# Kernel tuning notes

Measured on AMD Instinct MI355X. Metric: run time of the kernel, lower is better.

Reference implementation:

```python
import jax, jax.numpy as jnp
import numpy as np

B = 4; C = 3; IMG = 256; P = 16; HP = 16; HW = 256
DIM = 512; DEPTH = 6; HEADS = 8; DH = 64
NS = 50; SH = 4; SDH = 64; ITERS = 3; RPD = 128; FF = 2048; N = NS + HW


def _ln(x, g, b):
    m = jnp.mean(x, -1, keepdims=True)
    v = jnp.var(x, -1, keepdims=True)
    return (x - m) * jax.lax.rsqrt(v + 1e-5) * g + b


def _rms(x, g):
    # lucidrains RMSNorm: F.normalize(x, dim=-1) * sqrt(dim) * gamma
    n = jnp.linalg.norm(x, axis=-1, keepdims=True)
    return x / jnp.maximum(n, 1e-12) * (DIM ** 0.5) * g


def setup_inputs() -> dict:
    key = jax.random.key(0)
    ks = iter(jax.random.split(key, 64))
    def W(*s):
        return jax.random.normal(next(ks), s, jnp.float32) * 0.02
    SI = SH * SDH
    d = {}
    d['images'] = jax.random.normal(next(ks), (B, C, IMG, IMG), jnp.float32)
    d['slot_noise'] = jax.random.normal(next(ks), (B, NS, DIM), jnp.float32)
    d['patch_w'] = W(C * P * P, DIM); d['patch_b'] = jnp.zeros((DIM,))
    d['hpos'] = W(HP, DIM); d['wpos'] = W(HP, DIM)
    d['rp_w1'] = W(2, RPD); d['rp_b1'] = jnp.zeros((RPD,))
    d['rp_w2'] = W(RPD, RPD); d['rp_b2'] = jnp.zeros((RPD,))
    d['rp_w3'] = W(RPD, HEADS); d['rp_b3'] = jnp.zeros((HEADS,))
    d['slots_mu'] = W(1, 1, DIM); d['slots_logsigma'] = jnp.zeros((1, 1, DIM))
    d['sa_ln_in_g'] = jnp.ones((DIM,)); d['sa_ln_in_b'] = jnp.zeros((DIM,))
    d['sa_ln_sl_g'] = jnp.ones((DIM,)); d['sa_ln_sl_b'] = jnp.zeros((DIM,))
    d['sa_wq'] = W(DIM, SI); d['sa_bq'] = jnp.zeros((SI,))
    d['sa_wk'] = W(DIM, SI); d['sa_bk'] = jnp.zeros((SI,))
    d['sa_wv'] = W(DIM, SI); d['sa_bv'] = jnp.zeros((SI,))
    d['sa_wo'] = W(SI, DIM); d['sa_bo'] = jnp.zeros((DIM,))
    d['gru_wih'] = W(DIM, 3 * DIM); d['gru_whh'] = W(DIM, 3 * DIM)
    d['gru_bih'] = jnp.zeros((3 * DIM,)); d['gru_bhh'] = jnp.zeros((3 * DIM,))
    d['sa_ln_ff_g'] = jnp.ones((DIM,)); d['sa_ln_ff_b'] = jnp.zeros((DIM,))
    d['sa_mlp_w1'] = W(DIM, DIM); d['sa_mlp_b1'] = jnp.zeros((DIM,))
    d['sa_mlp_w2'] = W(DIM, DIM); d['sa_mlp_b2'] = jnp.zeros((DIM,))
    d['s2c_w'] = W(DIM, 2); d['s2c_b'] = jnp.zeros((2,))
    d['attn_g'] = jnp.ones((DEPTH, DIM))
    d['wq'] = W(DEPTH, DIM, HEADS * DH); d['wk'] = W(DEPTH, DIM, HEADS * DH)
    d['wv'] = W(DEPTH, DIM, HEADS * DH); d['wo'] = W(DEPTH, HEADS * DH, DIM)
    d['ff_g'] = jnp.ones((DEPTH, DIM))
    d['ff_w1'] = W(DEPTH, DIM, FF); d['ff_b1'] = jnp.zeros((DEPTH, FF))
    d['ff_w2'] = W(DEPTH, FF, DIM); d['ff_b2'] = jnp.zeros((DEPTH, DIM))
    d['final_g'] = jnp.ones((DIM,))
    d['pred_w'] = W(DIM, DIM); d['pred_b'] = jnp.zeros((DIM,))
    return d


def reference(images, slot_noise, patch_w, patch_b, hpos, wpos,
              rp_w1, rp_b1, rp_w2, rp_b2, rp_w3, rp_b3,
              slots_mu, slots_logsigma, sa_ln_in_g, sa_ln_in_b, sa_ln_sl_g, sa_ln_sl_b,
              sa_wq, sa_bq, sa_wk, sa_bk, sa_wv, sa_bv, sa_wo, sa_bo,
              gru_wih, gru_whh, gru_bih, gru_bhh, sa_ln_ff_g, sa_ln_ff_b,
              sa_mlp_w1, sa_mlp_b1, sa_mlp_w2, sa_mlp_b2, s2c_w, s2c_b,
              attn_g, wq, wk, wv, wo, ff_g, ff_w1, ff_b1, ff_w2, ff_b2,
              final_g, pred_w, pred_b):
    b = images.shape[0]
    # patchify: b c (h p1) (w p2) -> b h w (p1 p2 c)
    x = images.reshape(b, C, HP, P, HP, P).transpose(0, 2, 4, 3, 5, 1).reshape(b, HP, HP, P * P * C)
    tokens = x @ patch_w + patch_b                     # [b, HP, HP, DIM]
    tokens = tokens + hpos[:, None, :] + wpos[None, :, :]
    tokens = tokens.reshape(b, HW, DIM)
    # --- multi-head slot attention ---
    inp = _ln(tokens, sa_ln_in_g, sa_ln_in_b)
    k = (inp @ sa_wk + sa_bk).reshape(b, HW, SH, SDH).transpose(0, 2, 1, 3)
    v = (inp @ sa_wv + sa_bv).reshape(b, HW, SH, SDH).transpose(0, 2, 1, 3)
    slots = slots_mu + jnp.exp(slots_logsigma) * slot_noise  # [b, NS, DIM]
    scale = SDH ** -0.5
    for _ in range(ITERS):
        prev = slots
        s = _ln(slots, sa_ln_sl_g, sa_ln_sl_b)
        q = (s @ sa_wq + sa_bq).reshape(b, NS, SH, SDH).transpose(0, 2, 1, 3)
        dots = jnp.einsum('bhid,bhjd->bhij', q, k) * scale     # [b, SH, NS, HW]
        attn = jax.nn.softmax(dots, axis=-2) + 1e-8            # softmax over slots
        attn = attn / jnp.sum(attn, -1, keepdims=True)         # weighted mean over inputs
        upd = jnp.einsum('bhij,bhjd->bhid', attn, v)
        upd = upd.transpose(0, 2, 1, 3).reshape(b, NS, SH * SDH) @ sa_wo + sa_bo
        # GRUCell(updates, prev_slots)
        gx = upd @ gru_wih + gru_bih
        gh = prev @ gru_whh + gru_bhh
        xr, xz, xn = jnp.split(gx, 3, -1)
        hr, hz, hn = jnp.split(gh, 3, -1)
        r = jax.nn.sigmoid(xr + hr)
        z = jax.nn.sigmoid(xz + hz)
        nn_ = jnp.tanh(xn + r * hn)
        slots = (1 - z) * nn_ + z * prev
        slots = slots + (jax.nn.relu(_ln(slots, sa_ln_ff_g, sa_ln_ff_b) @ sa_mlp_w1 + sa_mlp_b1) @ sa_mlp_w2 + sa_mlp_b2)
    objects = slots
    slot_coords = objects @ s2c_w + s2c_b              # [b, NS, 2]
    # --- relative position MLP bias (slots coords + patch grid) ---
    g = jnp.arange(HP, dtype=jnp.float32)
    grid = jnp.stack(jnp.meshgrid(g, g, indexing='ij'), -1).reshape(HW, 2)
    coords = jnp.concatenate([slot_coords, jnp.broadcast_to(grid, (b, HW, 2))], axis=1)  # [b, N, 2]
    rel = coords[:, :, None, :] - coords[:, None, :, :]   # [b, N, N, 2]
    hmid = jax.nn.silu(rel @ rp_w1 + rp_b1)
    hmid = jax.nn.silu(hmid @ rp_w2 + rp_b2)
    bias = jnp.transpose(hmid @ rp_w3 + rp_b3, (0, 3, 1, 2))  # [b, HEADS, N, N]
    # --- transformer with per-layer rel-pos bias ---
    x = jnp.concatenate([objects, tokens], axis=1)     # [b, N, DIM]
    ascale = DH ** -0.5
    for l in range(DEPTH):
        h = _rms(x, attn_g[l])
        qh = (h @ wq[l]).reshape(b, N, HEADS, DH).transpose(0, 2, 1, 3)
        kh = (h @ wk[l]).reshape(b, N, HEADS, DH).transpose(0, 2, 1, 3)
        vh = (h @ wv[l]).reshape(b, N, HEADS, DH).transpose(0, 2, 1, 3)
        sim = jnp.einsum('bhid,bhjd->bhij', qh, kh) * ascale + bias
        a = jax.nn.softmax(sim, -1)
        o = jnp.einsum('bhij,bhjd->bhid', a, vh).transpose(0, 2, 1, 3).reshape(b, N, HEADS * DH) @ wo[l]
        x = x + o
        h = _rms(x, ff_g[l])
        x = x + (jax.nn.gelu(h @ ff_w1[l] + ff_b1[l]) @ ff_w2[l] + ff_b2[l])
    x = _rms(x, final_g)
    return x[:, NS:] @ pred_w + pred_b                 # [b, HW, DIM]
```

## Files before the change

kernel.cpp:

```cpp
#include <hip/hip_runtime.h>
#include <hip/hip_bf16.h>

typedef __hip_bfloat16 bf16;
typedef short short8v __attribute__((ext_vector_type(8)));
typedef float float4v __attribute__((ext_vector_type(4)));

static __device__ __forceinline__ float b2f(bf16 x){ return __bfloat162float(x); }

static __device__ __forceinline__ float ldin(const void* p, size_t i, bool isbf) {
  return isbf ? b2f(((const bf16*)p)[i]) : ((const float*)p)[i];
}

static __device__ __forceinline__ unsigned short f2bu(float f) {
  bf16 h = __float2bfloat16(f);
  return *reinterpret_cast<unsigned short*>(&h);
}

#define CDIV(a,b) (((a)+(b)-1)/(b))

#define NB   4
#define NSL  50
#define HWT  256
#define NT   306
#define DIM  512
// ... 46 lines not shown
  __shared__ unsigned short S[64 * 72];
  int t = threadIdx.x;
  int kk = t >> 4, nn = (t & 15) * 4;
#pragma unroll
  for (int r = 0; r < 4; ++r) {
    int k = k0 + kk + r * 16;
    unsigned short v[4];
    if (isbf) {
      ushort4 u = *(const ushort4*)((const unsigned short*)W + slice + (size_t)k * N + n0 + nn);
      v[0]=u.x; v[1]=u.y; v[2]=u.z; v[3]=u.w;
    } else {
      float4 f = *(const float4*)((const float*)W + slice + (size_t)k * N + n0 + nn);
      v[0]=f2bu(f.x); v[1]=f2bu(f.y); v[2]=f2bu(f.z); v[3]=f2bu(f.w);
    }
#pragma unroll
    for (int i = 0; i < 4; ++i) S[(nn + i) * 72 + kk + r * 16] = v[i];
  }
  __syncthreads();
  int nr = t >> 2, kc = (t & 3) * 16;
  short8v s0 = *(const short8v*)&S[nr * 72 + kc];
  short8v s1 = *(const short8v*)&S[nr * 72 + kc + 8];
  unsigned short* dst = dst0 + slice + (size_t)(n0 + nr) * K + k0 + kc;
  *(short8v*)dst = s0;
  *(short8v*)(dst + 8) = s1;
}

#define LDK 72
static __device__ __forceinline__ void gemm_body2(
    const void* __restrict__ A, int aty,
    const unsigned short* __restrict__ WT,
    const void* __restrict__ bias, size_t boff,
    void* __restrict__ C, int oty,
    int M, int N, int K, int kbeg, int kend,
    int act, int mode, bool isbf)
{
  __shared__ unsigned short As[64 * LDK];
  __shared__ unsigned short Bs[64 * LDK];
  const int tid = threadIdx.x;
  const int lane = tid & 63, wave = tid >> 6;
  const int quad = lane >> 4, ti = lane & 15;
  const int wm = (wave & 1) * 32, wn = (wave >> 1) * 32;
  const int bm = blockIdx.y * 64, bn = blockIdx.x * 64;
  const int srow = tid >> 2, sch = (tid & 3) * 16;

  unsigned short ha[16], hb[16];
  const int gm = bm + srow;
  const bool aok = gm < M;
  const unsigned short* Abf = (const unsigned short*)A + (size_t)gm * K;
  const float*          Af  = (const float*)A + (size_t)gm * K;
  const unsigned short* Bp  = WT + (size_t)(bn + srow) * K;

  auto fetchA = [&](int k0) {
    if (aok) {
      if (aty) {
        const ushort4* ap = (const ushort4*)(Abf + k0 + sch);
#pragma unroll
        for (int i = 0; i < 4; ++i) {
          ushort4 u = ap[i];
          ha[i*4+0]=u.x; ha[i*4+1]=u.y; ha[i*4+2]=u.z; ha[i*4+3]=u.w;
        }
      } else {
        const float4* ap = (const float4*)(Af + k0 + sch);
#pragma unroll
        for (int i = 0; i < 4; ++i) {
          float4 f = ap[i];
          ha[i*4+0]=f2bu(f.x); ha[i*4+1]=f2bu(f.y); ha[i*4+2]=f2bu(f.z); ha[i*4+3]=f2bu(f.w);
        }
// ... 25 lines not shown
    for (int ks = 0; ks < 2; ++ks) {
      short8v a0 = *reinterpret_cast<const short8v*>(&As[(wm + ti)      * LDK + ks * 32 + quad * 8]);
      short8v a1 = *reinterpret_cast<const short8v*>(&As[(wm + 16 + ti) * LDK + ks * 32 + quad * 8]);
      short8v b0 = *reinterpret_cast<const short8v*>(&Bs[(wn + ti)      * LDK + ks * 32 + quad * 8]);
      short8v b1 = *reinterpret_cast<const short8v*>(&Bs[(wn + 16 + ti) * LDK + ks * 32 + quad * 8]);
      acc00 = __builtin_amdgcn_mfma_f32_16x16x32_bf16(a0, b0, acc00, 0, 0, 0);
      acc01 = __builtin_amdgcn_mfma_f32_16x16x32_bf16(a0, b1, acc01, 0, 0, 0);
      acc10 = __builtin_amdgcn_mfma_f32_16x16x32_bf16(a1, b0, acc10, 0, 0, 0);
      acc11 = __builtin_amdgcn_mfma_f32_16x16x32_bf16(a1, b1, acc11, 0, 0, 0);
    }
    __syncthreads();
  }

  float4v accs[2][2] = {{acc00, acc01}, {acc10, acc11}};
#pragma unroll
  for (int mi = 0; mi < 2; ++mi) {
#pragma unroll
    for (int ni = 0; ni < 2; ++ni) {
      int row0 = bm + wm + mi * 16 + quad * 4;
      int col  = bn + wn + ni * 16 + ti;
      float bv = (bias && kbeg == 0) ? ldin(bias, boff + col, isbf) : 0.f;
#pragma unroll
      for (int r = 0; r < 4; ++r) {
        int row = row0 + r;
        if (row >= M) continue;
        float v = accs[mi][ni][r] + bv;
        if (act == 1) v = fmaxf(v, 0.f);
        else if (act == 2) {
          float u = 0.7978845608028654f * (v + 0.044715f * v * v * v);
          v = 0.5f * v * (1.f + tanhf(u));
        } else if (act == 3) {
          v = v / (1.f + expf(-v));
        }
        size_t idx = (size_t)row * N + col;
        if (oty) ((bf16*)C)[idx] = __float2bfloat16(v);
        else {
          float* Cf = (float*)C;
          if (mode == 2) atomicAdd(&Cf[idx], v);
          else if (mode == 1) Cf[idx] += v;
          else Cf[idx] = v;
        }
      }
    }
  }
}

__global__ __launch_bounds__(256) void gemm_mfma(
    const void* A, int aty, const unsigned short* WT, size_t woff,
    const void* bias, size_t boff, void* C, int oty,
    int M, int N, int K, int act, int accum, int zsplit, const int* __restrict__ flagp)
{
  int ksz = K / zsplit;
  int kbeg = blockIdx.z * ksz;
  int mode = zsplit > 1 ? 2 : (accum ? 1 : 0);
  gemm_body2(A, aty, WT + woff, bias, boff, C, oty, M, N, K, kbeg, kbeg + ksz,
             act, mode, *flagp != 0);
}

__global__ __launch_bounds__(256) void gemm_mfma_tri(
    const void* A, int aty, const unsigned short* WT, size_t o0, size_t o1, size_t o2,
    void* C0, void* C1, void* C2, int oty, int M, int N, int K,
    const int* __restrict__ flagp)
{
  size_t o = blockIdx.z == 0 ? o0 : (blockIdx.z == 1 ? o1 : o2);
  void* C = blockIdx.z == 0 ? C0 : (blockIdx.z == 1 ? C1 : C2);
  gemm_body2(A, aty, WT + o, nullptr, 0, C, oty, M, N, K, 0, K, 0, 0, *flagp != 0);
}

__global__ __launch_bounds__(256) void gemm_mfma_duo(
    const void* A0, const void* A1, int aty, const unsigned short* WT, size_t o0, size_t o1,
    const void* bias0, const void* bias1, void* C0, void* C1, int oty,
    int M, int N, int K, const int* __restrict__ flagp)
{
  const void* A = blockIdx.z ? A1 : A0;
  size_t o = blockIdx.z ? o1 : o0;
  const void* bias = blockIdx.z ? bias1 : bias0;
  void* C = blockIdx.z ? C1 : C0;
  gemm_body2(A, aty, WT + o, bias, 0, C, oty, M, N, K, 0, K, 0, 0, *flagp != 0);
}

__global__ void s2c_k(const float* __restrict__ slots, const void* __restrict__ w,
                      const void* __restrict__ bv, float* __restrict__ sc,
                      const int* __restrict__ flagp) {
  const bool isbf = *flagp != 0;
  int row = blockIdx.x, t = threadIdx.x;
  const float* x = slots + (size_t)row * DIM;
  float v0 = x[t], v1 = x[t + 256];
  float a0 = v0 * ldin(w, 2 * t, isbf)     + v1 * ldin(w, 2 * (t + 256), isbf);
  float a1 = v0 * ldin(w, 2 * t + 1, isbf) + v1 * ldin(w, 2 * (t + 256) + 1, isbf);
  __shared__ float r0[256], r1[256];
  r0[t] = a0; r1[t] = a1;
  __syncthreads();
  for (int o = 128; o > 0; o >>= 1) {
    if (t < o) { r0[t] += r0[t + o]; r1[t] += r1[t + o]; }
    __syncthreads();
  }
  if (t == 0) {
    sc[row * 2]     = r0[0] + ldin(bv, 0, isbf);
    sc[row * 2 + 1] = r1[0] + ldin(bv, 1, isbf);
  }
}

__global__ void patchify_k(const void* __restrict__ img, unsigned short* __restrict__ xp,
                           const int* __restrict__ flagp) {
  const bool isbf = *flagp != 0;
  int i = blockIdx.x * 256 + threadIdx.x;
  if (i >= NB * HWT * 768) return;
  int col = i % 768, row = i / 768;
  int c = col % 3, p2 = (col / 3) & 15, p1 = col / 48;
  int w = row & 15, h = (row >> 4) & 15, b = row >> 8;
  xp[i] = f2bu(ldin(img, (((size_t)(b * 3 + c) * 256 + h * 16 + p1) * 256) + w * 16 + p2, isbf));
}

__global__ void addpos_k(float* __restrict__ tok, const void* __restrict__ hp,
                         const void* __restrict__ wp, const int* __restrict__ flagp) {
  const bool isbf = *flagp != 0;
  int i = blockIdx.x * 256 + threadIdx.x;
  if (i >= NB * HWT * DIM) return;
  int d = i & 511;
  int row = i >> 9;
  int w = row & 15, h = (row >> 4) & 15;
  tok[i] += ldin(hp, h * DIM + d, isbf) + ldin(wp, w * DIM + d, isbf);
}

__global__ void ln512_k(const float* __restrict__ X, const void* __restrict__ g,
                        const void* __restrict__ b, unsigned short* __restrict__ Y,
                        const int* __restrict__ flagp) {
  const bool isbf = *flagp != 0;
  int row = blockIdx.x, t = threadIdx.x;
  const float* x = X + (size_t)row * DIM;
  float v0 = x[t], v1 = x[t + 256];
  __shared__ float rs[256], rq[256];
  rs[t] = v0 + v1; rq[t] = v0 * v0 + v1 * v1;
  __syncthreads();
  for (int o = 128; o > 0; o >>= 1) {
    if (t < o) { rs[t] += rs[t + o]; rq[t] += rq[t + o]; }
    __syncthreads();
  }
  float mean = rs[0] * (1.f / 512.f);
  float var  = rq[0] * (1.f / 512.f) - mean * mean;
  float inv  = rsqrtf(var + 1e-5f);
  unsigned short* y = Y + (size_t)row * DIM;
  y[t]       = f2bu((v0 - mean) * inv * ldin(g, t, isbf)       + ldin(b, t, isbf));
  y[t + 256] = f2bu((v1 - mean) * inv * ldin(g, t + 256, isbf) + ldin(b, t + 256, isbf));
}

__global__ void rms512_k(const float* __restrict__ X, const void* __restrict__ g,
                         int goff, unsigned short* __restrict__ Y, const int* __restrict__ flagp) {
  const bool isbf = *flagp != 0;
  int row = blockIdx.x, t = threadIdx.x;
  const float* x = X + (size_t)row * DIM;
  float v0 = x[t], v1 = x[t + 256];
  __shared__ float rq[256];
  rq[t] = v0 * v0 + v1 * v1;
  __syncthreads();
  for (int o = 128; o > 0; o >>= 1) {
    if (t < o) rq[t] += rq[t + o];
    __syncthreads();
  }
  float nrm = sqrtf(rq[0]);
  float sc = 22.62741699796952f / fmaxf(nrm, 1e-12f);
  unsigned short* y = Y + (size_t)row * DIM;
  y[t]       = f2bu(v0 * sc * ldin(g, goff + t, isbf));
  y[t + 256] = f2bu(v1 * sc * ldin(g, goff + t + 256, isbf));
}

__global__ void slots_init_k(const void* __restrict__ mu, const void* __restrict__ ls,
                             const void* __restrict__ noise, float* __restrict__ slots,
                             const int* __restrict__ flagp) {
  const bool isbf = *flagp != 0;
  int i = blockIdx.x * 256 + threadIdx.x;
  if (i >= NB * NSL * DIM) return;
  int d = i & 511;
  slots[i] = ldin(mu, d, isbf) + expf(ldin(ls, d, isbf)) * ldin(noise, i, isbf);
}

__global__ void slot_dots_k(const float* __restrict__ q, const float* __restrict__ k,
                            float* __restrict__ dots) {
  int blk = blockIdx.x;
  int i = blk % 50, h = (blk / 50) & 3, b = blk / 200;
  int j = threadIdx.x;
  __shared__ float qs[64];
  if (threadIdx.x < 64) qs[threadIdx.x] = q[((size_t)(b * 50 + i)) * 256 + h * 64 + threadIdx.x];
  __syncthreads();
  const float* kr = k + ((size_t)(b * 256 + j)) * 256 + h * 64;
  float s = 0.f;
#pragma unroll 8
  for (int d = 0; d < 64; ++d) s = fmaf(qs[d], kr[d], s);
  dots[(((size_t)(b * 4 + h) * 50) + i) * 256 + j] = s * 0.125f;
}

__global__ void softmax_slots_k(float* __restrict__ dots) {
  int idx = blockIdx.x * 256 + threadIdx.x;
  if (idx >= 4096) return;
  int j = idx & 255, h = (idx >> 8) & 3, b = idx >> 10;
  float* base = dots + ((size_t)(b * 4 + h) * 50) * 256 + j;
  float m = -1e30f;
  for (int i = 0; i < 50; ++i) m = fmaxf(m, base[i * 256]);
  float s = 0.f;
  for (int i = 0; i < 50; ++i) { float e = expf(base[i * 256] - m); base[i * 256] = e; s += e; }
  float inv = 1.f / s;
  for (int i = 0; i < 50; ++i) base[i * 256] *= inv;
}

__global__ void renorm_attn_k(float* __restrict__ attn) {
  int t = threadIdx.x;
  float* row = attn + (size_t)blockIdx.x * 256;
  float v = row[t] + 1e-8f;
  __shared__ float rs[256];
  rs[t] = v;
  __syncthreads();
  for (int o = 128; o > 0; o >>= 1) {
    if (t < o) rs[t] += rs[t + o];
    __syncthreads();
  }
  row[t] = v / rs[0];
}

__global__ void slot_upd_k(const float* __restrict__ attn, const float* __restrict__ v,
                           float* __restrict__ upd) {
  int bi = blockIdx.x;
  int b = bi / 50, i = bi % 50;
  int t = threadIdx.x, h = t >> 6;
  const float* arow = attn + ((size_t)((b * 4 + h) * 50) + i) * 256;
  float s = 0.f;
  for (int j = 0; j < 256; ++j) s = fmaf(arow[j], v[((size_t)(b * 256 + j)) * 256 + t], s);
  upd[(size_t)bi * 256 + t] = s;
}

__global__ void gru_k(const float* __restrict__ gx, const float* __restrict__ gh,
                      float* __restrict__ slots) {
  int i = blockIdx.x * 256 + threadIdx.x;
  if (i >= NB * NSL * DIM) return;
  int row = i >> 9, d = i & 511;
  size_t b3 = (size_t)row * 1536;
  float xr = gx[b3 + d], xz = gx[b3 + 512 + d], xn = gx[b3 + 1024 + d];
  float hr = gh[b3 + d], hz = gh[b3 + 512 + d], hn = gh[b3 + 1024 + d];
  float r = 1.f / (1.f + expf(-(xr + hr)));
  float z = 1.f / (1.f + expf(-(xz + hz)));
  float n = tanhf(xn + r * hn);
  float prev = slots[i];
  slots[i] = (1.f - z) * n + z * prev;
}

__global__ void build_coords_k(const float* __restrict__ sc, float* __restrict__ coords) {
  int i = blockIdx.x * 256 + threadIdx.x;
  if (i >= NB * NT) return;
  int b = i / NT, n = i % NT;
  float cx, cy;
  if (n < NSL) { cx = sc[(b * NSL + n) * 2]; cy = sc[(b * NSL + n) * 2 + 1]; }
  else { int t = n - NSL; cx = (float)(t >> 4); cy = (float)(t & 15); }
  coords[i * 2] = cx; coords[i * 2 + 1] = cy;
}

__global__ void relpos_table_k(const void* w1, const void* b1, const void* w2,
                               const void* b2, const void* w3, const void* b3,
                               float* __restrict__ tab, const int* __restrict__ flagp) {
  const bool isbf = *flagp != 0;
  int blk = blockIdx.x;
  float r0 = (float)(blk / 31 - 15), r1 = (float)(blk % 31 - 15);
  int t = threadIdx.x;
  __shared__ float h1[128], h2[128];
  float a = fmaf(r0, ldin(w1, t, isbf), fmaf(r1, ldin(w1, 128 + t, isbf), ldin(b1, t, isbf)));
  h1[t] = a / (1.f + expf(-a));
  __syncthreads();
  float s = ldin(b2, t, isbf);
#pragma unroll 4
  for (int k = 0; k < 128; ++k) s = fmaf(h1[k], ldin(w2, k * 128 + t, isbf), s);
  h2[t] = s / (1.f + expf(-s));
  __syncthreads();
  if (t < 8) {
    float o = ldin(b3, t, isbf);
#pragma unroll 4
    for (int k = 0; k < 128; ++k) o = fmaf(h2[k], ldin(w3, k * 8 + t, isbf), o);
    tab[blk * 8 + t] = o;
  }
}

__global__ void bias_fill_k(const float* __restrict__ tab, float* __restrict__ bias) {
  int i = blockIdx.x * 256 + threadIdx.x;
  if (i >= NB * NH * HWT * HWT) return;
  int jj = i & 255, ii = (i >> 8) & 255, h = (i >> 16) & 7, b = i >> 19;
  int di = (ii >> 4) - (jj >> 4) + 15;
  int dj = (ii & 15) - (jj & 15) + 15;
  bias[(((size_t)(b * NH + h) * NT) + NSL + ii) * NT + NSL + jj] = tab[(di * 31 + dj) * 8 + h];
}

__global__ void rp_l1_k(const float* __restrict__ coords, const void* w1, const void* b1,
                        unsigned short* __restrict__ H, int pbase, int pcount,
                        const int* __restrict__ flagp) {
  const bool isbf = *flagp != 0;
  int idx = blockIdx.x * 256 + threadIdx.x;
  if (idx >= pcount * 128) return;
  int pl = idx >> 7, u = idx & 127;
  int p = pbase + pl;
  int q = p % RPP, bb = p / RPP;
  int ii, jj;
  rp_decode(q, ii, jj);
  float r0 = coords[(bb * NT + ii) * 2]     - coords[(bb * NT + jj) * 2];
  float r1 = coords[(bb * NT + ii) * 2 + 1] - coords[(bb * NT + jj) * 2 + 1];
  float a = fmaf(r0, ldin(w1, u, isbf), fmaf(r1, ldin(w1, 128 + u, isbf), ldin(b1, u, isbf)));
  H[(size_t)pl * 128 + u] = f2bu(a / (1.f + expf(-a)));
}

__global__ __launch_bounds__(256) void rp_l3_k(
    const unsigned short* __restrict__ H2, const void* w3, const void* b3,
    float* __restrict__ bias, int pbase, int pcount, const int* __restrict__ flagp) {
  const bool isbf = *flagp != 0;
  __shared__ float W3s[128 * 8];
  int t = threadIdx.x;
  for (int e = t; e < 1024; e += 256) W3s[e] = ldin(w3, e, isbf);
  __syncthreads();
  int pl = blockIdx.x * 32 + (t >> 3), hh = t & 7;
  if (pl >= pcount) return;
  int p = pbase + pl;
  int q = p % RPP, bb = p / RPP;
  int ii, jj;
  rp_decode(q, ii, jj);
  float s = ldin(b3, hh, isbf);
  const unsigned short* hrow = H2 + (size_t)pl * 128;
#pragma unroll 8
  for (int k = 0; k < 128; ++k) {
    bf16 hv = *reinterpret_cast<const bf16*>(&hrow[k]);
    s = fmaf(b2f(hv), W3s[k * 8 + hh], s);
  }
  bias[((size_t)(bb * NH + hh) * NT + ii) * NT + jj] = s;
}

__global__ void build_x_k(const float* __restrict__ slots, const float* __restrict__ tok,
                          float* __restrict__ x) {
  int i = blockIdx.x * 256 + threadIdx.x;
  if (i >= NB * NT * DIM) return;
  int d = i & 511, n = (i >> 9) % NT, b = i / (NT * DIM);
  x[i] = (n < NSL) ? slots[((size_t)(b * NSL + n)) * DIM + d]
                   : tok[((size_t)(b * HWT + (n - NSL))) * DIM + d];
}

__global__ __launch_bounds__(256) void attn_fused_k(
    const unsigned short* __restrict__ Qb, const unsigned short* __restrict__ Kb,
    const unsigned short* __restrict__ Vb, const float* __restrict__ bias,
    unsigned short* __restrict__ Ob)
{
  const int bh = blockIdx.y, b = bh >> 3, h = bh & 7;
  const int i0 = blockIdx.x * 32;
  __shared__ unsigned short Qs[32 * 72];
  __shared__ unsigned short Ks[64 * 72];
  __shared__ float S[32 * 332];
  unsigned short* P = (unsigned short*)S;

  const int tid = threadIdx.x;
  const int lane = tid & 63, wave = tid >> 6, quad = lane >> 4, ti = lane & 15;
  const int mi = wave & 1, nh = wave >> 1;

  {
    int r = tid >> 3, c = (tid & 7) * 8;
    int gi = i0 + r;
    ushort4 u0 = {0,0,0,0}, u1 = {0,0,0,0};
// ... 83 lines not shown
          ushort4 u = p[i];
          hv[i*4+0]=u.x; hv[i*4+1]=u.y; hv[i*4+2]=u.z; hv[i*4+3]=u.w;
        }
      } else {
#pragma unroll
        for (int i = 0; i < 16; ++i) hv[i] = 0;
      }
#pragma unroll
      for (int i = 0; i < 16; ++i) Ks[(d0 + i) * 72 + key] = hv[i];
    }
    __syncthreads();
#pragma unroll
    for (int ntl = 0; ntl < 2; ++ntl) {
      int nt = nh * 2 + ntl;
#pragma unroll
      for (int ks = 0; ks < 2; ++ks) {
        short8v a  = *(const short8v*)&P[(mi * 16 + ti) * 664 + vt * 64 + ks * 32 + quad * 8];
        short8v bb = *(const short8v*)&Ks[(nt * 16 + ti) * 72 + ks * 32 + quad * 8];
        oacc[ntl] = __builtin_amdgcn_mfma_f32_16x16x32_bf16(a, bb, oacc[ntl], 0, 0, 0);
      }
    }
  }

#pragma unroll
  for (int ntl = 0; ntl < 2; ++ntl) {
    int dim = nh * 32 + ntl * 16 + ti;
#pragma unroll
    for (int r = 0; r < 4; ++r) {
      int row_g = i0 + mi * 16 + quad * 4 + r;
      if (row_g < NT)
        Ob[((size_t)(b * NT + row_g)) * DIM + h * 64 + dim] = f2bu(oacc[ntl][r]);
    }
  }
}

__global__ void write_out_k(const float* __restrict__ tmp, void* __restrict__ out,
                            const int* __restrict__ flagp) {
  const bool isbf = *flagp != 0;
  int i = blockIdx.x * 256 + threadIdx.x;
  if (i >= NB * HWT * DIM) return;
  int d = i & 511, tt = (i >> 9) & 255, b = i / (HWT * DIM);
  float v = tmp[((size_t)(b * NT + NSL + tt)) * DIM + d];
  if (isbf) ((bf16*)out)[i] = __float2bfloat16(v);
  else      ((float*)out)[i] = v;
}

extern "C" void kernel_launch(void* const* d_in, const int* in_sizes, int n_in,
                              void* d_out, int out_size, void* d_ws, size_t ws_size,
                              hipStream_t stream) {
  const void* images        = d_in[0];
  const void* slot_noise    = d_in[1];
  const void* patch_w       = d_in[2];
  const void* patch_b       = d_in[3];
  const void* hpos          = d_in[4];
  const void* wpos          = d_in[5];
  const void* rp_w1         = d_in[6];
  const void* rp_b1         = d_in[7];
  const void* rp_w2         = d_in[8];
  const void* rp_b2         = d_in[9];
  const void* rp_w3         = d_in[10];
  const void* rp_b3         = d_in[11];
  const void* slots_mu      = d_in[12];
  const void* slots_logsig  = d_in[13];
  const void* sa_ln_in_g    = d_in[14];
  const void* sa_ln_in_b    = d_in[15];
  const void* sa_ln_sl_g    = d_in[16];
  const void* sa_ln_sl_b    = d_in[17];
  const void* sa_wq         = d_in[18];
  const void* sa_bq         = d_in[19];
  const void* sa_wk         = d_in[20];
  const void* sa_bk         = d_in[21];
  const void* sa_wv         = d_in[22];
  const void* sa_bv         = d_in[23];
  const void* sa_wo         = d_in[24];
  const void* sa_bo         = d_in[25];
  const void* gru_wih       = d_in[26];
  const void* gru_whh       = d_in[27];
// ... 22 lines not shown
  const void* pred_b        = d_in[50];

  float* ws = (float*)d_ws;
  int* FLAG = (int*)ws;
  size_t off = 16;
  auto alloc = [&](size_t n) { float* p = ws + off; off += (n + 15) & ~(size_t)15; return p; };
  float* TOK   = alloc((size_t)NB * HWT * DIM);
  unsigned short* INPB = (unsigned short*)alloc((size_t)NB * HWT * DIM / 2);
  float* KB    = alloc((size_t)NB * HWT * 256);
  float* VB    = alloc((size_t)NB * HWT * 256);
  float* SLOTS = alloc((size_t)NB * NSL * DIM);
  unsigned short* SLNB = (unsigned short*)alloc((size_t)NB * NSL * DIM / 2);
  float* QB    = alloc((size_t)NB * NSL * 256);
  float* ATT   = alloc((size_t)NB * 4 * NSL * HWT);
  float* UPD   = alloc((size_t)NB * NSL * 256);
  float* UPDP  = alloc((size_t)NB * NSL * DIM);
  unsigned short* HIDSB = (unsigned short*)alloc((size_t)NB * NSL * DIM / 2);
  float* SC    = alloc((size_t)NB * NSL * 2);
  float* CRD   = alloc((size_t)NB * NT * 2);
  float* TAB   = alloc((size_t)961 * 8);
  float* BIAS  = alloc((size_t)NB * NH * NT * NT);
  float* X     = alloc((size_t)NB * NT * DIM);
  unsigned short* HBB  = (unsigned short*)alloc((size_t)NB * NT * DIM / 2);
  unsigned short* QHB  = (unsigned short*)alloc((size_t)NB * NT * DIM / 2);
  unsigned short* KHB  = (unsigned short*)alloc((size_t)NB * NT * DIM / 2);
  unsigned short* VHB  = (unsigned short*)alloc((size_t)NB * NT * DIM / 2);
  float* SIM   = alloc((size_t)NB * NH * NT * NT);
  unsigned short* OBB  = (unsigned short*)alloc((size_t)NB * NT * DIM / 2);
  unsigned short* FFHB = (unsigned short*)alloc((size_t)NB * NT * FF / 2);
  float* OUTT  = alloc((size_t)NB * NT * DIM);
  unsigned short* XPB = (unsigned short*)OUTT;
  float* GX = SIM;
  float* GH = SIM + (size_t)NB * NSL * 1536;
  const size_t oPatch = 0;
  const size_t oKw    = oPatch + (size_t)512 * 768;
  const size_t oVw    = oKw    + (size_t)256 * 512;
  const size_t oQw    = oVw    + (size_t)256 * 512;
  const size_t oWo    = oQw    + (size_t)256 * 512;
  const size_t oGih   = oWo    + (size_t)512 * 256;
  const size_t oGhh   = oGih   + (size_t)1536 * 512;
  const size_t oMlp1  = oGhh   + (size_t)1536 * 512;
  const size_t oMlp2  = oMlp1  + (size_t)512 * 512;
  const size_t oRp2   = oMlp2  + (size_t)512 * 512;
  const size_t oWq    = oRp2   + (size_t)128 * 128;
  const size_t oWk    = oWq    + (size_t)6 * 512 * 512;
  const size_t oWv    = oWk    + (size_t)6 * 512 * 512;
  const size_t oWol   = oWv    + (size_t)6 * 512 * 512;
  const size_t oFf1   = oWol   + (size_t)6 * 512 * 512;
  const size_t oFf2   = oFf1   + (size_t)6 * 512 * 2048;
  const size_t oPred  = oFf2   + (size_t)6 * 2048 * 512;
  const size_t wtTotal = oPred + (size_t)512 * 512;
  unsigned short* WTS = (unsigned short*)alloc((wtTotal + 1) / 2);
  (void)ws_size; (void)in_sizes; (void)n_in; (void)out_size;

#define GEMMM(A_, ATY_, WOFF_, BIAS_, BOFF_, C_, OTY_, M_, N_, K_, ACT_, ACC_, ZS_) \
  gemm_mfma<<<dim3((N_)/64, CDIV((M_),64), (ZS_)), 256, 0, stream>>>( \
      A_, ATY_, WTS, (size_t)(WOFF_), BIAS_, (size_t)(BOFF_), C_, OTY_, M_, N_, K_, ACT_, ACC_, ZS_, FLAG)

  const int MROW = NB * NT;
  const int MS   = NB * NSL;

  detect_k<<<1, 256, 0, stream>>>(images, FLAG);
  {
    WtArgs a;
    const void* Wp[17] = { patch_w, sa_wk, sa_wv, sa_wq, sa_wo, gru_wih, gru_whh,
                           sa_mlp_w1, sa_mlp_w2, rp_w2, wq, wk, wv, wo, ff_w1, ff_w2, pred_w };
    const size_t Oo[17] = { oPatch, oKw, oVw, oQw, oWo, oGih, oGhh,
                            oMlp1, oMlp2, oRp2, oWq, oWk, oWv, oWol, oFf1, oFf2, oPred };
    const int Kk[17] = {768,512,512,512,256,512,512,512,512,128,512,512,512,512,512,2048,512};
    const int Nn[17] = {512,256,256,256,512,1536,1536,512,512,128,512,512,512,512,2048,512,512};
    const int Ll[17] = {1,1,1,1,1,1,1,1,1,1,6,6,6,6,6,6,1};
    int acc = 0;
    for (int i = 0; i < 17; ++i) {
      a.W[i] = Wp[i]; a.wto[i] = Oo[i]; a.K[i] = Kk[i]; a.N[i] = Nn[i];
      a.base[i] = acc;
      acc += Ll[i] * (Kk[i] >> 6) * (Nn[i] >> 6);
    }
    a.base[17] = acc;
    wtrans_all_k<<<acc, 256, 0, stream>>>(a, WTS, FLAG);
  }

  patchify_k<<<CDIV(NB*HWT*768, 256), 256, 0, stream>>>(images, XPB, FLAG);
  hipMemsetAsync(TOK, 0, (size_t)NB * HWT * DIM * sizeof(float), stream);
  GEMMM(XPB, 1, oPatch, patch_b, 0, TOK, 0, NB*HWT, DIM, 768, 0, 0, 3);
  addpos_k<<<CDIV(NB*HWT*DIM, 256), 256, 0, stream>>>(TOK, hpos, wpos, FLAG);

  ln512_k<<<NB*HWT, 256, 0, stream>>>(TOK, sa_ln_in_g, sa_ln_in_b, INPB, FLAG);
  gemm_mfma_duo<<<dim3(4, 16, 2), 256, 0, stream>>>(
      INPB, INPB, 1, WTS, oKw, oVw, sa_bk, sa_bv, KB, VB, 0, NB*HWT, 256, DIM, FLAG);
  slots_init_k<<<CDIV(NB*NSL*DIM, 256), 256, 0, stream>>>(slots_mu, slots_logsig, slot_noise, SLOTS, FLAG);

  for (int it = 0; it < 3; ++it) {
    ln512_k<<<MS, 256, 0, stream>>>(SLOTS, sa_ln_sl_g, sa_ln_sl_b, SLNB, FLAG);
    GEMMM(SLNB, 1, oQw, sa_bq, 0, QB, 0, MS, 256, DIM, 0, 0, 1);
    slot_dots_k<<<NB*4*NSL, 256, 0, stream>>>(QB, KB, ATT);
    softmax_slots_k<<<16, 256, 0, stream>>>(ATT);
    renorm_attn_k<<<NB*4*NSL, 256, 0, stream>>>(ATT);
    slot_upd_k<<<MS, 256, 0, stream>>>(ATT, VB, UPD);
    GEMMM(UPD, 0, oWo, sa_bo, 0, UPDP, 0, MS, DIM, 256, 0, 0, 1);
    gemm_mfma_duo<<<dim3(24, 4, 2), 256, 0, stream>>>(
        UPDP, SLOTS, 0, WTS, oGih, oGhh, gru_bih, gru_bhh, GX, GH, 0, MS, 1536, DIM, FLAG);
    gru_k<<<CDIV(NB*NSL*DIM, 256), 256, 0, stream>>>(GX, GH, SLOTS);
    ln512_k<<<MS, 256, 0, stream>>>(SLOTS, sa_ln_ff_g, sa_ln_ff_b, SLNB, FLAG);
    GEMMM(SLNB, 1, oMlp1, sa_mlp_b1, 0, HIDSB, 1, MS, DIM, DIM, 1, 0, 1);
    GEMMM(HIDSB, 1, oMlp2, sa_mlp_b2, 0, SLOTS, 0, MS, DIM, DIM, 0, 1, 1);
  }

  s2c_k<<<MS, 256, 0, stream>>>(SLOTS, s2c_w, s2c_b, SC, FLAG);
  build_coords_k<<<CDIV(NB*NT, 256), 256, 0, stream>>>(SC, CRD);
  relpos_table_k<<<961, 128, 0, stream>>>(rp_w1, rp_b1, rp_w2, rp_b2, rp_w3, rp_b3, TAB, FLAG);
  bias_fill_k<<<CDIV(NB*NH*HWT*HWT, 256), 256, 0, stream>>>(TAB, BIAS);
  {
    unsigned short* H1 = HBB;
    unsigned short* H2 = HBB + (size_t)PCH * 128;
    for (int c = 0; c < 2; ++c) {
      int pb = c * PCH;
      rp_l1_k<<<CDIV(PCH*128, 256), 256, 0, stream>>>(CRD, rp_w1, rp_b1, H1, pb, PCH, FLAG);
      GEMMM(H1, 1, oRp2, rp_b2, 0, H2, 1, PCH, 128, 128, 3, 0, 1);
      rp_l3_k<<<CDIV(PCH,32), 256, 0, stream>>>(H2, rp_w3, rp_b3, BIAS, pb, PCH, FLAG);
    }
  }

  build_x_k<<<CDIV(NB*NT*DIM, 256), 256, 0, stream>>>(SLOTS, TOK, X);
  for (int l = 0; l < 6; ++l) {
    size_t lw = (size_t)l * 512 * 512;
    rms512_k<<<MROW, 256, 0, stream>>>(X, attn_g, l * DIM, HBB, FLAG);
    gemm_mfma_tri<<<dim3(8, 20, 3), 256, 0, stream>>>(
        HBB, 1, WTS, oWq + lw, oWk + lw, oWv + lw, QHB, KHB, VHB, 1, MROW, DIM, DIM, FLAG);
    attn_fused_k<<<dim3(10, NB*NH), 256, 0, stream>>>(QHB, KHB, VHB, BIAS, OBB);
    GEMMM(OBB, 1, oWol + lw, (const void*)nullptr, 0, X, 0, MROW, DIM, DIM, 0, 1, 2);
    rms512_k<<<MROW, 256, 0, stream>>>(X, ff_g, l * DIM, HBB, FLAG);
    GEMMM(HBB, 1, oFf1 + (size_t)l * 512 * 2048, ff_b1, l * FF, FFHB, 1, MROW, FF, DIM, 2, 0, 1);
    GEMMM(FFHB, 1, oFf2 + (size_t)l * 2048 * 512, ff_b2, l * DIM, X, 0, MROW, DIM, FF, 0, 1, 4);
  }

  rms512_k<<<MROW, 256, 0, stream>>>(X, final_g, 0, HBB, FLAG);
  hipMemsetAsync(OUTT, 0, (size_t)NB * NT * DIM * sizeof(float), stream);
  GEMMM(HBB, 1, oPred, pred_b, 0, OUTT, 0, MROW, DIM, DIM, 0, 0, 2);
  write_out_k<<<CDIV(NB*HWT*DIM, 256), 256, 0, stream>>>(OUTT, d_out, FLAG);

#undef GEMMM
}
```

Baseline: 1.173 ms.

## Fuse slot attention, pos-add, coords and output scatter into fewer kernels

Measured after the change: 1.395 ms. 1.19x slower.

```diff
diff --git a/kernel.cpp b/kernel.cpp
--- a/kernel.cpp
+++ b/kernel.cpp
@@ -102,7 +102,9 @@
     const void* __restrict__ bias, size_t boff,
     void* __restrict__ C, int oty,
     int M, int N, int K, int kbeg, int kend,
-    int act, int mode, bool isbf)
+    int act, int mode, int spec,
+    const void* __restrict__ p0, const void* __restrict__ p1,
+    bool isbf)
 {
   __shared__ unsigned short As[64 * LDK];
   __shared__ unsigned short Bs[64 * LDK];
@@ -194,13 +196,26 @@
         } else if (act == 3) {
           v = v / (1.f + expf(-v));
         }
-        size_t idx = (size_t)row * N + col;
-        if (oty) ((bf16*)C)[idx] = __float2bfloat16(v);
-        else {
-          float* Cf = (float*)C;
-          if (mode == 2) atomicAdd(&Cf[idx], v);
-          else if (mode == 1) Cf[idx] += v;
-          else Cf[idx] = v;
+        if (spec == 2 && kbeg == 0) {
+          int hh = (row >> 4) & 15, ww = row & 15;
+          v += ldin(p0, hh * N + col, isbf) + ldin(p1, ww * N + col, isbf);
+        }
+        if (spec == 1) {
+          int b_ = row / NT, n_ = row % NT;
+          if (n_ >= NSL) {
+            size_t oi = ((size_t)(b_ * HWT + (n_ - NSL))) * N + col;
+            if (isbf) ((bf16*)C)[oi] = __float2bfloat16(v);
+            else      ((float*)C)[oi] = v;
+          }
+        } else {
+          size_t idx = (size_t)row * N + col;
+          if (oty) ((bf16*)C)[idx] = __float2bfloat16(v);
+          else {
+            float* Cf = (float*)C;
+            if (mode == 2) atomicAdd(&Cf[idx], v);
+            else if (mode == 1) Cf[idx] += v;
+            else Cf[idx] = v;
+          }
         }
       }
     }
@@ -210,13 +225,14 @@
 __global__ __launch_bounds__(256) void gemm_mfma(
     const void* A, int aty, const unsigned short* WT, size_t woff,
     const void* bias, size_t boff, void* C, int oty,
-    int M, int N, int K, int act, int accum, int zsplit, const int* __restrict__ flagp)
+    int M, int N, int K, int act, int accum, int zsplit,
+    int spec, const void* p0, const void* p1, const int* __restrict__ flagp)
 {
   int ksz = K / zsplit;
   int kbeg = blockIdx.z * ksz;
   int mode = zsplit > 1 ? 2 : (accum ? 1 : 0);
   gemm_body2(A, aty, WT + woff, bias, boff, C, oty, M, N, K, kbeg, kbeg + ksz,
-             act, mode, *flagp != 0);
+             act, mode, spec, p0, p1, *flagp != 0);
 }
 
 __global__ __launch_bounds__(256) void gemm_mfma_tri(
@@ -226,7 +242,8 @@
 {
   size_t o = blockIdx.z == 0 ? o0 : (blockIdx.z == 1 ? o1 : o2);
   void* C = blockIdx.z == 0 ? C0 : (blockIdx.z == 1 ? C1 : C2);
-  gemm_body2(A, aty, WT + o, nullptr, 0, C, oty, M, N, K, 0, K, 0, 0, *flagp != 0);
+  gemm_body2(A, aty, WT + o, nullptr, 0, C, oty, M, N, K, 0, K, 0, 0, 0,
+             nullptr, nullptr, *flagp != 0);
 }
 
 __global__ __launch_bounds__(256) void gemm_mfma_duo(
@@ -238,28 +255,40 @@
   size_t o = blockIdx.z ? o1 : o0;
   const void* bias = blockIdx.z ? bias1 : bias0;
   void* C = blockIdx.z ? C1 : C0;
-  gemm_body2(A, aty, WT + o, bias, 0, C, oty, M, N, K, 0, K, 0, 0, *flagp != 0);
-}
-
-__global__ void s2c_k(const float* __restrict__ slots, const void* __restrict__ w,
-                      const void* __restrict__ bv, float* __restrict__ sc,
-                      const int* __restrict__ flagp) {
+  gemm_body2(A, aty, WT + o, bias, 0, C, oty, M, N, K, 0, K, 0, 0, 0,
+             nullptr, nullptr, *flagp != 0);
+}
+
+__global__ void coords_k(const float* __restrict__ slots, const void* __restrict__ w,
+                         const void* __restrict__ bv, float* __restrict__ coords,
+                         const int* __restrict__ flagp) {
   const bool isbf = *flagp != 0;
-  int row = blockIdx.x, t = threadIdx.x;
-  const float* x = slots + (size_t)row * DIM;
-  float v0 = x[t], v1 = x[t + 256];
-  float a0 = v0 * ldin(w, 2 * t, isbf)     + v1 * ldin(w, 2 * (t + 256), isbf);
-  float a1 = v0 * ldin(w, 2 * t + 1, isbf) + v1 * ldin(w, 2 * (t + 256) + 1, isbf);
   __shared__ float r0[256], r1[256];
-  r0[t] = a0; r1[t] = a1;
-  __syncthreads();
-  for (int o = 128; o > 0; o >>= 1) {
-    if (t < o) { r0[t] += r0[t + o]; r1[t] += r1[t + o]; }
-    __syncthreads();
-  }
-  if (t == 0) {
-    sc[row * 2]     = r0[0] + ldin(bv, 0, isbf);
-    sc[row * 2 + 1] = r1[0] + ldin(bv, 1, isbf);
+  int blk = blockIdx.x, t = threadIdx.x;
+  if (blk < 200) {
+    int b = blk / 50, n = blk % 50;
+    const float* x = slots + (size_t)blk * DIM;
+    float v0 = x[t], v1 = x[t + 256];
+    float a0 = v0 * ldin(w, 2 * t, isbf)     + v1 * ldin(w, 2 * (t + 256), isbf);
+    float a1 = v0 * ldin(w, 2 * t + 1, isbf) + v1 * ldin(w, 2 * (t + 256) + 1, isbf);
+    r0[t] = a0; r1[t] = a1;
+    __syncthreads();
+    for (int o = 128; o > 0; o >>= 1) {
+      if (t < o) { r0[t] += r0[t + o]; r1[t] += r1[t + o]; }
+      __syncthreads();
+    }
+    if (t == 0) {
+      coords[((size_t)b * NT + n) * 2]     = r0[0] + ldin(bv, 0, isbf);
+      coords[((size_t)b * NT + n) * 2 + 1] = r1[0] + ldin(bv, 1, isbf);
+    }
+  } else {
+#pragma unroll
+    for (int s = 0; s < 4; ++s) {
+      int i = t + 256 * s;
+      int b = i >> 8, tt = i & 255;
+      coords[((size_t)b * NT + NSL + tt) * 2]     = (float)(tt >> 4);
+      coords[((size_t)b * NT + NSL + tt) * 2 + 1] = (float)(tt & 15);
+    }
   }
 }
 
@@ -274,17 +303,6 @@
   xp[i] = f2bu(ldin(img, (((size_t)(b * 3 + c) * 256 + h * 16 + p1) * 256) + w * 16 + p2, isbf));
 }
 
-__global__ void addpos_k(float* __restrict__ tok, const void* __restrict__ hp,
-                         const void* __restrict__ wp, const int* __restrict__ flagp) {
-  const bool isbf = *flagp != 0;
-  int i = blockIdx.x * 256 + threadIdx.x;
-  if (i >= NB * HWT * DIM) return;
-  int d = i & 511;
-  int row = i >> 9;
-  int w = row & 15, h = (row >> 4) & 15;
-  tok[i] += ldin(hp, h * DIM + d, isbf) + ldin(wp, w * DIM + d, isbf);
-}
-
 __global__ void ln512_k(const float* __restrict__ X, const void* __restrict__ g,
                         const void* __restrict__ b, unsigned short* __restrict__ Y,
                         const int* __restrict__ flagp) {
@@ -337,57 +355,89 @@
   slots[i] = ldin(mu, d, isbf) + expf(ldin(ls, d, isbf)) * ldin(noise, i, isbf);
 }
 
-__global__ void slot_dots_k(const float* __restrict__ q, const float* __restrict__ k,
-                            float* __restrict__ dots) {
-  int blk = blockIdx.x;
-  int i = blk % 50, h = (blk / 50) & 3, b = blk / 200;
-  int j = threadIdx.x;
-  __shared__ float qs[64];
-  if (threadIdx.x < 64) qs[threadIdx.x] = q[((size_t)(b * 50 + i)) * 256 + h * 64 + threadIdx.x];
-  __syncthreads();
-  const float* kr = k + ((size_t)(b * 256 + j)) * 256 + h * 64;
-  float s = 0.f;
-#pragma unroll 8
-  for (int d = 0; d < 64; ++d) s = fmaf(qs[d], kr[d], s);
-  dots[(((size_t)(b * 4 + h) * 50) + i) * 256 + j] = s * 0.125f;
-}
-
-__global__ void softmax_slots_k(float* __restrict__ dots) {
-  int idx = blockIdx.x * 256 + threadIdx.x;
-  if (idx >= 4096) return;
-  int j = idx & 255, h = (idx >> 8) & 3, b = idx >> 10;
-  float* base = dots + ((size_t)(b * 4 + h) * 50) * 256 + j;
-  float m = -1e30f;
-  for (int i = 0; i < 50; ++i) m = fmaxf(m, base[i * 256]);
-  float s = 0.f;
-  for (int i = 0; i < 50; ++i) { float e = expf(base[i * 256] - m); base[i * 256] = e; s += e; }
-  float inv = 1.f / s;
-  for (int i = 0; i < 50; ++i) base[i * 256] *= inv;
-}
-
-__global__ void renorm_attn_k(float* __restrict__ attn) {
-  int t = threadIdx.x;
-  float* row = attn + (size_t)blockIdx.x * 256;
-  float v = row[t] + 1e-8f;
-  __shared__ float rs[256];
-  rs[t] = v;
-  __syncthreads();
-  for (int o = 128; o > 0; o >>= 1) {
-    if (t < o) rs[t] += rs[t + o];
-    __syncthreads();
-  }
-  row[t] = v / rs[0];
-}
-
-__global__ void slot_upd_k(const float* __restrict__ attn, const float* __restrict__ v,
-                           float* __restrict__ upd) {
-  int bi = blockIdx.x;
-  int b = bi / 50, i = bi % 50;
-  int t = threadIdx.x, h = t >> 6;
-  const float* arow = attn + ((size_t)((b * 4 + h) * 50) + i) * 256;
-  float s = 0.f;
-  for (int j = 0; j < 256; ++j) s = fmaf(arow[j], v[((size_t)(b * 256 + j)) * 256 + t], s);
-  upd[(size_t)bi * 256 + t] = s;
+__global__ __launch_bounds__(256) void slot_attn_k(
+    const float* __restrict__ q, const float* __restrict__ k,
+    const float* __restrict__ v, float* __restrict__ upd)
+{
+  __shared__ float Qs[NSL * 64];
+  __shared__ float S[NSL * 257];
+  const int bh = blockIdx.x, b = bh >> 2, h = bh & 3;
+  const int t = threadIdx.x;
+
+  for (int e = t; e < NSL * 64; e += 256) {
+    int i = e >> 6, d = e & 63;
+    Qs[e] = q[((size_t)(b * NSL + i)) * 256 + h * 64 + d];
+  }
+  __syncthreads();
+
+  {
+    const float* kr = k + ((size_t)(b * HWT + t)) * 256 + h * 64;
+    float kreg[64];
+#pragma unroll
+    for (int d4 = 0; d4 < 16; ++d4) {
+      float4 f = *(const float4*)(kr + d4 * 4);
+      kreg[d4*4+0]=f.x; kreg[d4*4+1]=f.y; kreg[d4*4+2]=f.z; kreg[d4*4+3]=f.w;
+    }
+#pragma unroll 1
+    for (int i = 0; i < NSL; ++i) {
+      float s = 0.f;
+#pragma unroll
+      for (int d = 0; d < 64; ++d) s = fmaf(Qs[i * 64 + d], kreg[d], s);
+      S[i * 257 + t] = s * 0.125f;
+    }
+    float m = -1e30f;
+#pragma unroll 1
+    for (int i = 0; i < NSL; ++i) m = fmaxf(m, S[i * 257 + t]);
+    float ssum = 0.f;
+#pragma unroll 1
+    for (int i = 0; i < NSL; ++i) {
+      float e = __expf(S[i * 257 + t] - m);
+      S[i * 257 + t] = e; ssum += e;
+    }
+    float inv = 1.f / ssum;
+#pragma unroll 1
+    for (int i = 0; i < NSL; ++i) S[i * 257 + t] = fmaf(S[i * 257 + t], inv, 1e-8f);
+  }
+  __syncthreads();
+
+  {
+    const int w = t >> 6, l = t & 63;
+    for (int i = w; i < NSL; i += 4) {
+      float a0 = S[i * 257 + l],       a1 = S[i * 257 + 64 + l];
+      float a2 = S[i * 257 + 128 + l], a3 = S[i * 257 + 192 + l];
+      float s4 = a0 + a1 + a2 + a3;
+#pragma unroll
+      for (int o = 1; o < 64; o <<= 1) s4 += __shfl_xor(s4, o);
+      float inv2 = 1.f / s4;
+      S[i * 257 + l]       = a0 * inv2;
+      S[i * 257 + 64 + l]  = a1 * inv2;
+      S[i * 257 + 128 + l] = a2 * inv2;
+      S[i * 257 + 192 + l] = a3 * inv2;
+    }
+  }
+  __syncthreads();
+
+  {
+    const int d = t & 63, g = t >> 6;
+    float acc[13];
+#pragma unroll
+    for (int r = 0; r < 13; ++r) acc[r] = 0.f;
+    const float* vbase = v + ((size_t)(b * HWT)) * 256 + h * 64 + d;
+#pragma unroll 1
+    for (int j = 0; j < HWT; ++j) {
+      float vv = vbase[(size_t)j * 256];
+#pragma unroll
+      for (int r = 0; r < 13; ++r) {
+        int i = g + 4 * r;
+        if (i < NSL) acc[r] = fmaf(S[i * 257 + j], vv, acc[r]);
+      }
+    }
+#pragma unroll
+    for (int r = 0; r < 13; ++r) {
+      int i = g + 4 * r;
+      if (i < NSL) upd[((size_t)(b * NSL + i)) * 256 + h * 64 + d] = acc[r];
+    }
+  }
 }
 
 __global__ void gru_k(const float* __restrict__ gx, const float* __restrict__ gh,
@@ -403,16 +453,6 @@
   float n = tanhf(xn + r * hn);
   float prev = slots[i];
   slots[i] = (1.f - z) * n + z * prev;
-}
-
-__global__ void build_coords_k(const float* __restrict__ sc, float* __restrict__ coords) {
-  int i = blockIdx.x * 256 + threadIdx.x;
-  if (i >= NB * NT) return;
-  int b = i / NT, n = i % NT;
-  float cx, cy;
-  if (n < NSL) { cx = sc[(b * NSL + n) * 2]; cy = sc[(b * NSL + n) * 2 + 1]; }
-  else { int t = n - NSL; cx = (float)(t >> 4); cy = (float)(t & 15); }
-  coords[i * 2] = cx; coords[i * 2 + 1] = cy;
 }
 
 __global__ void relpos_table_k(const void* w1, const void* b1, const void* w2,
@@ -469,9 +509,12 @@
     const unsigned short* __restrict__ H2, const void* w3, const void* b3,
     float* __restrict__ bias, int pbase, int pcount, const int* __restrict__ flagp) {
   const bool isbf = *flagp != 0;
-  __shared__ float W3s[128 * 8];
+  __shared__ float W3s[8 * 132];
   int t = threadIdx.x;
-  for (int e = t; e < 1024; e += 256) W3s[e] = ldin(w3, e, isbf);
+  for (int e = t; e < 1024; e += 256) {
+    int k = e >> 3, hh = e & 7;
+    W3s[hh * 132 + k] = ldin(w3, e, isbf);
+  }
   __syncthreads();
   int pl = blockIdx.x * 32 + (t >> 3), hh = t & 7;
   if (pl >= pcount) return;
@@ -481,10 +524,15 @@
   rp_decode(q, ii, jj);
   float s = ldin(b3, hh, isbf);
   const unsigned short* hrow = H2 + (size_t)pl * 128;
+  const float* wrow = &W3s[hh * 132];
 #pragma unroll 8
-  for (int k = 0; k < 128; ++k) {
-    bf16 hv = *reinterpret_cast<const bf16*>(&hrow[k]);
-    s = fmaf(b2f(hv), W3s[k * 8 + hh], s);
+  for (int k4 = 0; k4 < 32; ++k4) {
+    ushort4 h4 = *(const ushort4*)(hrow + k4 * 4);
+    float4  w4 = *(const float4*)(wrow + k4 * 4);
+    s = fmaf(b2f(*reinterpret_cast<bf16*>(&h4.x)), w4.x, s);
+    s = fmaf(b2f(*reinterpret_cast<bf16*>(&h4.y)), w4.y, s);
+    s = fmaf(b2f(*reinterpret_cast<bf16*>(&h4.z)), w4.z, s);
+    s = fmaf(b2f(*reinterpret_cast<bf16*>(&h4.w)), w4.w, s);
   }
   bias[((size_t)(bb * NH + hh) * NT + ii) * NT + jj] = s;
 }
@@ -634,17 +682,6 @@
         Ob[((size_t)(b * NT + row_g)) * DIM + h * 64 + dim] = f2bu(oacc[ntl][r]);
     }
   }
-}
-
-__global__ void write_out_k(const float* __restrict__ tmp, void* __restrict__ out,
-                            const int* __restrict__ flagp) {
-  const bool isbf = *flagp != 0;
-  int i = blockIdx.x * 256 + threadIdx.x;
-  if (i >= NB * HWT * DIM) return;
-  int d = i & 511, tt = (i >> 9) & 255, b = i / (HWT * DIM);
-  float v = tmp[((size_t)(b * NT + NSL + tt)) * DIM + d];
-  if (isbf) ((bf16*)out)[i] = __float2bfloat16(v);
-  else      ((float*)out)[i] = v;
 }
 
 extern "C" void kernel_launch(void* const* d_in, const int* in_sizes, int n_in,
@@ -733,6 +770,7 @@
   unsigned short* XPB = (unsigned short*)OUTT;
   float* GX = SIM;
   float* GH = SIM + (size_t)NB * NSL * 1536;
+  (void)ATT; (void)SC;
   const size_t oPatch = 0;
   const size_t oKw    = oPatch + (size_t)512 * 768;
   const size_t oVw    = oKw    + (size_t)256 * 512;
@@ -754,9 +792,10 @@
   unsigned short* WTS = (unsigned short*)alloc((wtTotal + 1) / 2);
   (void)ws_size; (void)in_sizes; (void)n_in; (void)out_size;
 
-#define GEMMM(A_, ATY_, WOFF_, BIAS_, BOFF_, C_, OTY_, M_, N_, K_, ACT_, ACC_, ZS_) \
+#define GEMMM(A_, ATY_, WOFF_, BIAS_, BOFF_, C_, OTY_, M_, N_, K_, ACT_, ACC_, ZS_, SPEC_, P0_, P1_) \
   gemm_mfma<<<dim3((N_)/64, CDIV((M_),64), (ZS_)), 256, 0, stream>>>( \
-      A_, ATY_, WTS, (size_t)(WOFF_), BIAS_, (size_t)(BOFF_), C_, OTY_, M_, N_, K_, ACT_, ACC_, ZS_, FLAG)
+      A_, ATY_, WTS, (size_t)(WOFF_), BIAS_, (size_t)(BOFF_), C_, OTY_, M_, N_, K_, ACT_, ACC_, ZS_, \
+      SPEC_, P0_, P1_, FLAG)
 
   const int MROW = NB * NT;
   const int MS   = NB * NSL;
@@ -783,8 +822,7 @@
 
   patchify_k<<<CDIV(NB*HWT*768, 256), 256, 0, stream>>>(images, XPB, FLAG);
   hipMemsetAsync(TOK, 0, (size_t)NB * HWT * DIM * sizeof(float), stream);
-  GEMMM(XPB, 1, oPatch, patch_b, 0, TOK, 0, NB*HWT, DIM, 768, 0, 0, 3);
-  addpos_k<<<CDIV(NB*HWT*DIM, 256), 256, 0, stream>>>(TOK, hpos, wpos, FLAG);
+  GEMMM(XPB, 1, oPatch, patch_b, 0, TOK, 0, NB*HWT, DIM, 768, 0, 0, 3, 2, hpos, wpos);
 
   ln512_k<<<NB*HWT, 256, 0, stream>>>(TOK, sa_ln_in_g, sa_ln_in_b, INPB, FLAG);
   gemm_mfma_duo<<<dim3(4, 16, 2), 256, 0, stream>>>(
@@ -793,22 +831,18 @@
 
   for (int it = 0; it < 3; ++it) {
     ln512_k<<<MS, 256, 0, stream>>>(SLOTS, sa_ln_sl_g, sa_ln_sl_b, SLNB, FLAG);
-    GEMMM(SLNB, 1, oQw, sa_bq, 0, QB, 0, MS, 256, DIM, 0, 0, 1);
-    slot_dots_k<<<NB*4*NSL, 256, 0, stream>>>(QB, KB, ATT);
-    softmax_slots_k<<<16, 256, 0, stream>>>(ATT);
-    renorm_attn_k<<<NB*4*NSL, 256, 0, stream>>>(ATT);
-    slot_upd_k<<<MS, 256, 0, stream>>>(ATT, VB, UPD);
-    GEMMM(UPD, 0, oWo, sa_bo, 0, UPDP, 0, MS, DIM, 256, 0, 0, 1);
+    GEMMM(SLNB, 1, oQw, sa_bq, 0, QB, 0, MS, 256, DIM, 0, 0, 1, 0, nullptr, nullptr);
+    slot_attn_k<<<16, 256, 0, stream>>>(QB, KB, VB, UPD);
+    GEMMM(UPD, 0, oWo, sa_bo, 0, UPDP, 0, MS, DIM, 256, 0, 0, 1, 0, nullptr, nullptr);
     gemm_mfma_duo<<<dim3(24, 4, 2), 256, 0, stream>>>(
         UPDP, SLOTS, 0, WTS, oGih, oGhh, gru_bih, gru_bhh, GX, GH, 0, MS, 1536, DIM, FLAG);
     gru_k<<<CDIV(NB*NSL*DIM, 256), 256, 0, stream>>>(GX, GH, SLOTS);
     ln512_k<<<MS, 256, 0, stream>>>(SLOTS, sa_ln_ff_g, sa_ln_ff_b, SLNB, FLAG);
-    GEMMM(SLNB, 1, oMlp1, sa_mlp_b1, 0, HIDSB, 1, MS, DIM, DIM, 1, 0, 1);
-    GEMMM(HIDSB, 1, oMlp2, sa_mlp_b2, 0, SLOTS, 0, MS, DIM, DIM, 0, 1, 1);
-  }
-
-  s2c_k<<<MS, 256, 0, stream>>>(SLOTS, s2c_w, s2c_b, SC, FLAG);
-  build_coords_k<<<CDIV(NB*NT, 256), 256, 0, stream>>>(SC, CRD);
+    GEMMM(SLNB, 1, oMlp1, sa_mlp_b1, 0, HIDSB, 1, MS, DIM, DIM, 1, 0, 1, 0, nullptr, nullptr);
+    GEMMM(HIDSB, 1, oMlp2, sa_mlp_b2, 0, SLOTS, 0, MS, DIM, DIM, 0, 1, 1, 0, nullptr, nullptr);
+  }
+
+  coords_k<<<201, 256, 0, stream>>>(SLOTS, s2c_w, s2c_b, CRD, FLAG);
   relpos_table_k<<<961, 128, 0, stream>>>(rp_w1, rp_b1, rp_w2, rp_b2, rp_w3, rp_b3, TAB, FLAG);
   bias_fill_k<<<CDIV(NB*NH*HWT*HWT, 256), 256, 0, stream>>>(TAB, BIAS);
   {
@@ -817,7 +851,7 @@
     for (int c = 0; c < 2; ++c) {
       int pb = c * PCH;
       rp_l1_k<<<CDIV(PCH*128, 256), 256, 0, stream>>>(CRD, rp_w1, rp_b1, H1, pb, PCH, FLAG);
-      GEMMM(H1, 1, oRp2, rp_b2, 0, H2, 1, PCH, 128, 128, 3, 0, 1);
+      GEMMM(H1, 1, oRp2, rp_b2, 0, H2, 1, PCH, 128, 128, 3, 0, 1, 0, nullptr, nullptr);
       rp_l3_k<<<CDIV(PCH,32), 256, 0, stream>>>(H2, rp_w3, rp_b3, BIAS, pb, PCH, FLAG);
     }
   }
@@ -829,16 +863,14 @@
     gemm_mfma_tri<<<dim3(8, 20, 3), 256, 0, stream>>>(
         HBB, 1, WTS, oWq + lw, oWk + lw, oWv + lw, QHB, KHB, VHB, 1, MROW, DIM, DIM, FLAG);
     attn_fused_k<<<dim3(10, NB*NH), 256, 0, stream>>>(QHB, KHB, VHB, BIAS, OBB);
-    GEMMM(OBB, 1, oWol + lw, (const void*)nullptr, 0, X, 0, MROW, DIM, DIM, 0, 1, 2);
+    GEMMM(OBB, 1, oWol + lw, (const void*)nullptr, 0, X, 0, MROW, DIM, DIM, 0, 1, 2, 0, nullptr, nullptr);
     rms512_k<<<MROW, 256, 0, stream>>>(X, ff_g, l * DIM, HBB, FLAG);
-    GEMMM(HBB, 1, oFf1 + (size_t)l * 512 * 2048, ff_b1, l * FF, FFHB, 1, MROW, FF, DIM, 2, 0, 1);
-    GEMMM(FFHB, 1, oFf2 + (size_t)l * 2048 * 512, ff_b2, l * DIM, X, 0, MROW, DIM, FF, 0, 1, 4);
+    GEMMM(HBB, 1, oFf1 + (size_t)l * 512 * 2048, ff_b1, l * FF, FFHB, 1, MROW, FF, DIM, 2, 0, 1, 0, nullptr, nullptr);
+    GEMMM(FFHB, 1, oFf2 + (size_t)l * 2048 * 512, ff_b2, l * DIM, X, 0, MROW, DIM, FF, 0, 1, 4, 0, nullptr, nullptr);
   }
 
   rms512_k<<<MROW, 256, 0, stream>>>(X, final_g, 0, HBB, FLAG);
-  hipMemsetAsync(OUTT, 0, (size_t)NB * NT * DIM * sizeof(float), stream);
-  GEMMM(HBB, 1, oPred, pred_b, 0, OUTT, 0, MROW, DIM, DIM, 0, 0, 2);
-  write_out_k<<<CDIV(NB*HWT*DIM, 256), 256, 0, stream>>>(OUTT, d_out, FLAG);
+  GEMMM(HBB, 1, oPred, pred_b, 0, d_out, 0, MROW, DIM, DIM, 0, 0, 1, 1, nullptr, nullptr);
 
 #undef GEMMM
 }
```
